# Kernel tuning notes

Hardware: AMD Instinct MI355X
Metric: run time of the kernel (lower is better)

## Reference

```python
import jax, jax.numpy as jnp
import numpy as np

N, C, T, V = 32, 64, 512, 25
CO = 64            # out_channels
C4 = CO // 4       # inter channel (conv_a/conv_d output, kc//3)
W3 = 3 * V         # unfolded node dim
BN_EPS = 1e-5


def setup_inputs() -> dict:
    key = jax.random.key(0)
    ks = jax.random.split(key, 12)
    s = 0.05
    return {
        "x": jax.random.normal(ks[0], (N, C, T, V), dtype=jnp.float32),
        "A": jax.random.uniform(ks[1], (3, W3, W3), dtype=jnp.float32) * 0.1,  # fixed adjacency buffer
        "PA": jnp.full((3, W3, W3), 1e-6, dtype=jnp.float32),                   # learned adjacency offset
        "conv_a_w": jax.random.normal(ks[2], (C4, C), dtype=jnp.float32) * s,   # 1x1 conv_a[0]
        "conv_a_b": jnp.zeros((C4,), dtype=jnp.float32),
        "conv_d_w": jax.random.normal(ks[3], (C4, C), dtype=jnp.float32) * s,   # 1x1 conv_d[0]
        "conv_d_b": jnp.zeros((C4,), dtype=jnp.float32),
        "conv_w": jax.random.normal(ks[4], (3 * C4, C), dtype=jnp.float32) * s, # main 1x1 conv (t_kernel_size=1)
        "conv_b": jnp.zeros((3 * C4,), dtype=jnp.float32),
        "out_w": jax.random.normal(ks[5], (CO, C4, 3), dtype=jnp.float32) * s,  # conv3d kernel (1,3,1)
        "out_b": jnp.zeros((CO,), dtype=jnp.float32),
        "bn_gamma": jnp.ones((CO,), dtype=jnp.float32),
        "bn_beta": jnp.zeros((CO,), dtype=jnp.float32),
        "bn_mean": jnp.zeros((CO,), dtype=jnp.float32),
        "bn_var": jnp.ones((CO,), dtype=jnp.float32),
    }


def _unfold3(x):
    # UnfoldTemporalWindows(3,1,1): (N,C,T,V) -> (N,C,T,3V), zero-pad T by 1
    n, c, t, v = x.shape
    xp = jnp.pad(x, ((0, 0), (0, 0), (1, 1), (0, 0)))
    win = jnp.stack([xp[:, :, i:i + t, :] for i in range(3)], axis=3)  # (N,C,T,3,V)
    return win.reshape(n, c, t, 3 * v)


def reference(x, A, PA, conv_a_w, conv_a_b, conv_d_w, conv_d_b,
              conv_w, conv_b, out_w, out_b, bn_gamma, bn_beta, bn_mean, bn_var):
    n, c, t, v = x.shape
    w3 = 3 * v
    Aeff = A + PA  # (3, 3V, 3V)

    x2 = _unfold3(x)  # (N,C,T,3V)

    # adaptive graph attention: matmul-softmax-matmul
    a1 = jnp.einsum('nctw,oc->notw', x2, conv_a_w) + conv_a_b[None, :, None, None]  # (N,C4,T,3V)
    a11 = a1.transpose(0, 3, 1, 2).reshape(n, w3, -1)   # (N,3V,C4*T)
    a2 = a1.reshape(n, -1, w3)                          # (N,C4*T,3V)
    att = jax.nn.softmax(jnp.matmul(a11, a2) / w3, axis=-2)  # (N,3V,3V), softmax over dim -2
    xz = jnp.matmul(x2.reshape(n, c * t, w3), att).reshape(n, c, t, w3)
    z = jnp.einsum('nctw,oc->notw', xz, conv_d_w) + conv_d_b[None, :, None, None]  # (N,C4,T,3V)

    # main branch: 1x1 conv -> split into k=3 -> einsum graph conv with A
    x1 = jnp.einsum('nctw,oc->notw', x2, conv_w) + conv_b[None, :, None, None]  # (N,3*C4,T,3V)
    c4 = conv_d_w.shape[0]
    x1 = x1.reshape(n, 3, c4, t, w3)
    x1 = jnp.einsum('nkctv,kvw->nctw', x1, Aeff)  # (N,C4,T,3V)
    x1 = x1 + z

    # conv3d (1,3,1) collapses the window-of-3 dim
    x1 = x1.reshape(n, c4, t, 3, v)
    y = jnp.einsum('nctwv,ocw->notv', x1, out_w) + out_b[None, :, None, None]  # (N,CO,T,V)

    # BatchNorm2d (inference form)
    inv = jax.lax.rsqrt(bn_var + BN_EPS)
    y = (y - bn_mean[None, :, None, None]) * (bn_gamma * inv)[None, :, None, None] + bn_beta[None, :, None, None]

    y = y + x  # in_channels == out_channels -> identity residual
    return jax.nn.relu(y)
```

## Files before the change

### kernel.cpp

```cpp
#include <hip/hip_runtime.h>
#include <hip/hip_bf16.h>


typedef unsigned short u16;
typedef unsigned int   u32;
typedef __attribute__((ext_vector_type(8))) short bf16x8;
typedef __attribute__((ext_vector_type(4))) float f32x4;

__device__ __forceinline__ float b2f(u32 u) {
    union { u32 i; float f; } x; x.i = (u & 0xffffu) << 16; return x.f;
}
__device__ __forceinline__ u16 f2b(float f) {
    union { float f; u32 i; } x; x.f = f;
    u32 i = x.i;
    return (u16)((i + 0x7fffu + ((i >> 16) & 1u)) >> 16);
}
__device__ __forceinline__ u32 pack2(float a, float b) {
    return (u32)f2b(a) | ((u32)f2b(b) << 16);
}
__device__ __forceinline__ void unpack8(uint4 u, float* f) {
    f[0] = b2f(u.x); f[1] = b2f(u.x >> 16);
    f[2] = b2f(u.y); f[3] = b2f(u.y >> 16);
    f[4] = b2f(u.z); f[5] = b2f(u.z >> 16);
    f[6] = b2f(u.w); f[7] = b2f(u.w >> 16);
}

__global__ __launch_bounds__(256) void k0_bta(
    const float* __restrict__ A, const float* __restrict__ PA,
    u16* __restrict__ BtA)
{
    int e = blockIdx.x * 256 + threadIdx.x;
    if (e >= 80 * 288) return;
    int w = e / 288, k = e - w * 288;
    int r = k >> 5, v = k & 31, g = r / 3, i = r - g * 3;
    float val = 0.f;
    if (v < 25 && w < 75) {
        int idx = (g * 75 + i * 25 + v) * 75 + w;
        val = A[idx] + PA[idx];
    }
    BtA[e] = f2b(val);
}

__global__ __launch_bounds__(256, 2) void k1_conv80(
    const float* __restrict__ x,
    const float* __restrict__ wa, const float* __restrict__ ba,
    const float* __restrict__ wd, const float* __restrict__ bd,
    const float* __restrict__ wc, const float* __restrict__ bc,
    u16* __restrict__ a1o, u16* __restrict__ hcn)
{
    __shared__ __align__(16) u16 Xt[256 * 64];
    __shared__ __align__(16) u16 Csh[80 * 264];
    char* XtB = (char*)Xt;

    const int b    = blockIdx.x;
    const int n    = b >> 4;
    const int t0   = (b & 15) << 5;
    const int tid  = threadIdx.x;
    const int wave = tid >> 6, lane = tid & 63;
    const int q    = lane >> 4, r = lane & 15;

    bf16x8 wfrag[5][2];
    float  breg[5];
    #pragma unroll
    for (int mt = 0; mt < 5; ++mt) {
        const int o = mt * 16 + r;
        const float* src = (o < 16) ? (wa + o * 64)
                         : (o < 32) ? (wd + (o - 16) * 64)
                                    : (wc + (o - 32) * 64);
        breg[mt] = (o < 16) ? ba[o] : (o < 32) ? bd[o - 16] : bc[o - 32];
        #pragma unroll
        for (int ks = 0; ks < 2; ++ks) {
            bf16x8 f;
            #pragma unroll
            for (int j = 0; j < 8; ++j)
                f[j] = (short)f2b(src[ks * 32 + q * 8 + j]);
            wfrag[mt][ks] = f;
        }
    }

    if (t0 == 0) {
        uint4 z; z.x = 0u; z.y = 0u; z.z = 0u; z.w = 0u;
        for (int e = tid; e < 50; e += 256)
            *(uint4*)&a1o[((size_t)n * 514) * 400 + e * 8] = z;
    }
    if (t0 == 480) {
        uint4 z; z.x = 0u; z.y = 0u; z.z = 0u; z.w = 0u;
        for (int e = tid; e < 50; e += 256)
            *(uint4*)&a1o[((size_t)n * 514 + 513) * 400 + e * 8] = z;
    }

    {
        uint4 z; z.x = 0u; z.y = 0u; z.z = 0u; z.w = 0u;
        for (int e = tid; e < 448; e += 256) {
            const int pc = e >> 3, ch = e & 7;
            const int tl = pc / 7, pv = pc - tl * 7;
            const int col = tl * 32 + 25 + pv;
            *(uint4*)(XtB + col * 128 + ch * 16) = z;
        }
    }

    auto epilogue = [&](int tbp) {
        for (int e = tid; e < 2048; e += 256) {
            const int cc  = e >> 5;
            const int rem = e & 31;
            const int tl  = rem >> 2, v0 = (rem & 3) << 3;
            const int o   = (cc < 48) ? cc + 32 : cc - 32;
            uint4 pk = *(const uint4*)&Csh[o * 264 + tl * 32 + v0];
            *(uint4*)&hcn[(((size_t)n * 64 + cc) * 512 + (tbp + tl)) * 32 + v0] = pk;
        }
        for (int e = tid; e < 400; e += 256) {
            const int tv = e >> 1, h = (e & 1) << 3;
            const int tl = (tv * 41) >> 10;
            const int v  = tv - tl * 25;
            const int cb = tl * 32 + v;
            u16 a[8];
            #pragma unroll
            for (int k = 0; k < 8; ++k) a[k] = Csh[(h + k) * 264 + cb];
            uint4 pk;
            pk.x = (u32)a[0] | ((u32)a[1] << 16);
            pk.y = (u32)a[2] | ((u32)a[3] << 16);
            pk.z = (u32)a[4] | ((u32)a[5] << 16);
            pk.w = (u32)a[6] | ((u32)a[7] << 16);
            *(uint4*)&a1o[(((size_t)n * 514 + (tbp + tl + 1)) * 25 + v) * 16 + h] = pk;
        }
    };

    for (int s = 0; s < 4; ++s) {
        const int tb = t0 + s * 8;

        if (s > 0) epilogue(tb - 8);
        for (int e = tid; e < 400; e += 256) {
            const int co = e / 50;
            const int tq = e - co * 50;
            const float* gp = x + (((size_t)n * 64 + co * 8) * 512 + tb) * 25 + tq * 4;
            float fl[32];
            #pragma unroll
            for (int i = 0; i < 8; ++i) {
                const float4 t4 = *(const float4*)(gp + (size_t)i * 12800);
                fl[i * 4 + 0] = t4.x; fl[i * 4 + 1] = t4.y;
                fl[i * 4 + 2] = t4.z; fl[i * 4 + 3] = t4.w;
            }
            #pragma unroll
            for (int j = 0; j < 4; ++j) {
                const int tv  = tq * 4 + j;
                const int tl  = (tv * 41) >> 10;
                const int col = tl * 32 + (tv - tl * 25);
                uint4 pk;
                pk.x = pack2(fl[0 * 4 + j], fl[1 * 4 + j]);
                pk.y = pack2(fl[2 * 4 + j], fl[3 * 4 + j]);
                pk.z = pack2(fl[4 * 4 + j], fl[5 * 4 + j]);
                pk.w = pack2(fl[6 * 4 + j], fl[7 * 4 + j]);
                *(uint4*)(XtB + col * 128 + ((co * 16) ^ ((col & 7) << 4))) = pk;
            }
        }
        __syncthreads();

        {
            f32x4 acc[4][5];
            #pragma unroll
            for (int a_ = 0; a_ < 4; ++a_)
                #pragma unroll
                for (int m_ = 0; m_ < 5; ++m_)
                    acc[a_][m_] = (f32x4){0.f, 0.f, 0.f, 0.f};

            #pragma unroll
            for (int nt4 = 0; nt4 < 4; ++nt4) {
                const int col = (wave * 4 + nt4) * 16 + r;
                const int swz = (col & 7) << 4;
                const char* rowp = (const char*)Xt + col * 128;
                const bf16x8 x0 = *(const bf16x8*)(rowp + ((q * 16) ^ swz));
                const bf16x8 x1 = *(const bf16x8*)(rowp + ((64 + q * 16) ^ swz));
                #pragma unroll
                for (int mt = 0; mt < 5; ++mt) {
                    acc[nt4][mt] = __builtin_amdgcn_mfma_f32_16x16x32_bf16(
                        x0, wfrag[mt][0], acc[nt4][mt], 0, 0, 0);
                    acc[nt4][mt] = __builtin_amdgcn_mfma_f32_16x16x32_bf16(
                        x1, wfrag[mt][1], acc[nt4][mt], 0, 0, 0);
                }
            }
            #pragma unroll
            for (int nt4 = 0; nt4 < 4; ++nt4) {
                const int colb = (wave * 4 + nt4) * 16 + q * 4;
                #pragma unroll
                for (int mt = 0; mt < 5; ++mt) {
                    const int o = mt * 16 + r;
                    const float bi = breg[mt];
                    uint2 pr;
                    pr.x = pack2(acc[nt4][mt][0] + bi, acc[nt4][mt][1] + bi);
                    pr.y = pack2(acc[nt4][mt][2] + bi, acc[nt4][mt][3] + bi);
                    *(uint2*)&Csh[o * 264 + colb] = pr;
                }
            }
        }
        __syncthreads();
    }
    epilogue(t0 + 24);
}

__global__ __launch_bounds__(256, 2) void k2a_mfma(
    const u16* __restrict__ a1o, float* __restrict__ Spart)
{
    __shared__ u16 U[80 * 136];
    __shared__ float Sred[80 * 80];
    const int b   = blockIdx.x;
    const int n   = b >> 4;
    const int tc  = b & 15;
    const int t0  = tc * 32;
    const int tid = threadIdx.x;
    const int wave = tid >> 6, lane = tid & 63;
    const int q = lane >> 4, col = lane & 15;

    f32x4 acc[25];
    #pragma unroll
    for (int i = 0; i < 25; ++i) acc[i] = (f32x4){0.f, 0.f, 0.f, 0.f};

    for (int s = 0; s < 4; ++s) {
        __syncthreads();
        for (int e = tid; e < 1280; e += 256) {
            int row = e >> 4, c8 = (e & 15) << 3;
            uint4 val; val.x = 0u; val.y = 0u; val.z = 0u; val.w = 0u;
            if (row < 75) {
                int i = row / 25, v = row - i * 25;
                int tl = c8 >> 4, o0 = c8 & 8;
                int tp = t0 + s * 8 + tl + i;
                val = *(const uint4*)&a1o[(((size_t)n * 514 + tp) * 25 + v) * 16 + o0];
            }
            *(uint4*)&U[row * 136 + c8] = val;
        }
        __syncthreads();

        const int k0 = wave * 32 + q * 8;
        bf16x8 fr[5];
        #pragma unroll
        for (int r = 0; r < 5; ++r)
            fr[r] = *(const bf16x8*)&U[(r * 16 + col) * 136 + k0];
        #pragma unroll
        for (int mt = 0; mt < 5; ++mt)
            #pragma unroll
            for (int nt = 0; nt < 5; ++nt)
                acc[mt * 5 + nt] = __builtin_amdgcn_mfma_f32_16x16x32_bf16(
                    fr[mt], fr[nt], acc[mt * 5 + nt], 0, 0, 0);
    }

    for (int w = 0; w < 4; ++w) {
        if (wave == w) {
            #pragma unroll
            for (int mt = 0; mt < 5; ++mt)
                #pragma unroll
                for (int nt = 0; nt < 5; ++nt)
                    #pragma unroll
                    for (int reg = 0; reg < 4; ++reg) {
                        int idx = (mt * 16 + q * 4 + reg) * 80 + nt * 16 + col;
                        if (w == 0) Sred[idx]  = acc[mt * 5 + nt][reg];
                        else        Sred[idx] += acc[mt * 5 + nt][reg];
                    }
        }
        __syncthreads();
    }
    float* dst = &Spart[(size_t)(n * 16 + tc) * 6400];
    for (int e = tid; e < 6400; e += 256) dst[e] = Sred[e];
}

__global__ __launch_bounds__(256) void k2b_softmax(
    const float* __restrict__ Spart, u16* __restrict__ BtT)
{
    __shared__ float S[6400];
    const int n = blockIdx.x, tid = threadIdx.x;
    for (int e = tid; e < 6400; e += 256) {
        float s = 0.f;
        for (int ks = 0; ks < 16; ++ks)
            s += Spart[(size_t)(n * 16 + ks) * 6400 + e];
        S[e] = s * (1.0f / 75.0f);
    }
    __syncthreads();
    if (tid < 80) {
        const int w2 = tid;
        float r = 0.f;
        if (w2 < 75) {
            float m = -1e30f;
            for (int w1 = 0; w1 < 75; ++w1) m = fmaxf(m, S[w1 * 80 + w2]);
            float s = 0.f;
            for (int w1 = 0; w1 < 75; ++w1) {
                float e = __expf(S[w1 * 80 + w2] - m);
                S[w1 * 80 + w2] = e;
                s += e;
            }
            r = 1.0f / s;
        }
        for (int k = 0; k < 96; ++k) {
            int i = k >> 5, v = k & 31;
            float val = (w2 < 75 && v < 25) ? S[(i * 25 + v) * 80 + w2] * r : 0.f;
            BtT[((size_t)n * 80 + w2) * 96 + k] = f2b(val);
        }
    }
}

__global__ __launch_bounds__(256, 2) void k3_graph(
    const u16* __restrict__ hcn, const u16* __restrict__ BtA,
    const u16* __restrict__ BtT, u16* __restrict__ sum12)
{
    __shared__ u16 Bt[80 * 392];
    const int b    = blockIdx.x;
    const int n    = b >> 4;
    const int tblk = (b & 15) << 5;
    const int tid  = threadIdx.x;

    for (int e = tid; e < 3840; e += 256) {
        int row = e / 48, cs = e - row * 48;
        uint4 val;
        if (cs < 36) val = *(const uint4*)&BtA[row * 288 + cs * 8];
        else         val = *(const uint4*)&BtT[((size_t)n * 80 + row) * 96 + (cs - 36) * 8];
        *(uint4*)&Bt[row * 392 + cs * 8] = val;
    }
    __syncthreads();

    const int wave = tid >> 6, lane = tid & 63;
    const int c = lane & 15, q = lane >> 4;
    const int tb = tblk + wave * 8;

    for (int tt = 0; tt < 8; tt += 2) {
        const int t0 = tb + tt, t1 = t0 + 1;
        bf16x8 a0[12], a1[12];
        #pragma unroll
        for (int r = 0; r < 12; ++r) {
            const int g = r / 3, i = r - g * 3;
            const size_t rowb = ((size_t)n * 64 + g * 16 + c) * 512;
            const int tp0 = t0 + i - 1, tp1 = t1 + i - 1;
            a0[r] = (tp0 >= 0 && tp0 < 512)
                  ? *(const bf16x8*)&hcn[(rowb + tp0) * 32 + q * 8] : (bf16x8)(short)0;
            a1[r] = (tp1 >= 0 && tp1 < 512)
                  ? *(const bf16x8*)&hcn[(rowb + tp1) * 32 + q * 8] : (bf16x8)(short)0;
        }
        #pragma unroll 1
        for (int nt = 0; nt < 5; ++nt) {
            f32x4 acc0 = {0.f, 0.f, 0.f, 0.f};
            f32x4 acc1 = {0.f, 0.f, 0.f, 0.f};
            const u16* bp = &Bt[(nt * 16 + c) * 392 + q * 8];
            #pragma unroll
            for (int r = 0; r < 12; ++r) {
                bf16x8 bf = *(const bf16x8*)(bp + r * 32);
                acc0 = __builtin_amdgcn_mfma_f32_16x16x32_bf16(a0[r], bf, acc0, 0, 0, 0);
                acc1 = __builtin_amdgcn_mfma_f32_16x16x32_bf16(a1[r], bf, acc1, 0, 0, 0);
            }
            const int w = nt * 16 + c;
            if (w < 75) {
                const int ww = (w >= 50) ? 2 : ((w >= 25) ? 1 : 0);
                const int v  = w - ww * 25;
                const size_t b0 = ((size_t)n * 512 + t0) * 1536 + v * 48 + q * 12 + ww;
                const size_t b1 = ((size_t)n * 512 + t1) * 1536 + v * 48 + q * 12 + ww;
                #pragma unroll
                for (int reg = 0; reg < 4; ++reg) {
                    sum12[b0 + (size_t)(reg * 3)] = f2b(acc0[reg]);
                    sum12[b1 + (size_t)(reg * 3)] = f2b(acc1[reg]);
                }
            }
        }
    }
}

__global__ __launch_bounds__(256, 2) void k4_out(
    const u16* __restrict__ sum12,
    const float* __restrict__ ow, const float* __restrict__ obias,
    const float* __restrict__ bg, const float* __restrict__ bb,
    const float* __restrict__ bm, const float* __restrict__ bv,
    const float* __restrict__ x, float* __restrict__ out)
{
    __shared__ __align__(16) u16 Bsh[256 * 64];
    char* BshB = (char*)Bsh;
    const int b    = blockIdx.x;
    const int n    = b >> 6;
    const int t0   = (b & 63) << 3;
    const int tid  = threadIdx.x;
    const int wave = tid >> 6, lane = tid & 63;
    const int q    = lane >> 4, c15 = lane & 15;

    {
        uint4 z; z.x = 0u; z.y = 0u; z.z = 0u; z.w = 0u;
        for (int e = tid; e < 960; e += 256) {
            int col, j;
            if (e < 512) { col = e >> 1; j = 6 + (e & 1); }
            else {
                const int r2 = e - 512;
                const int cc = r2 >> 3; j = r2 & 7;
                const int tl = cc / 7, pv = cc - tl * 7;
                col = tl * 32 + 25 + pv;
            }
            *(uint4*)(BshB + col * 128 + ((j * 16) ^ ((col & 7) << 4))) = z;
        }
    }
    for (int e = tid; e < 1200; e += 256) {
        const int j  = e % 6;
        const int rv = e / 6;
        const int tl = (rv * 41) >> 10;
        const int v  = rv - tl * 25;
        const uint4 val = *(const uint4*)
            &sum12[((size_t)n * 512 + t0 + tl) * 1536 + v * 48 + j * 8];
        const int col = tl * 32 + v;
        *(uint4*)(BshB + col * 128 + ((j * 16) ^ ((col & 7) << 4))) = val;
    }

    bf16x8 wfrag[4][2];
    #pragma unroll
    for (int mt = 0; mt < 4; ++mt) {
        const int o = mt * 16 + c15;
        #pragma unroll
        for (int ks = 0; ks < 2; ++ks) {
            bf16x8 f;
            #pragma unroll
            for (int j = 0; j < 8; ++j) {
                const int k = ks * 32 + q * 8 + j;
                f[j] = (k < 48) ? (short)f2b(ow[o * 48 + k]) : (short)0;
            }
            wfrag[mt][ks] = f;
        }
    }
    float scl[4][4], shf[4][4], obv[4][4];
    #pragma unroll
    for (int mt = 0; mt < 4; ++mt)
        #pragma unroll
        for (int reg = 0; reg < 4; ++reg) {
            const int o = mt * 16 + q * 4 + reg;
            const float s = bg[o] * rsqrtf(bv[o] + 1e-5f);
            scl[mt][reg] = s;
            shf[mt][reg] = bb[o] - bm[o] * s;
            obv[mt][reg] = obias[o];
        }
    __syncthreads();

    f32x4 acc[4][4];
    #pragma unroll
    for (int ct = 0; ct < 4; ++ct)
        #pragma unroll
        for (int mt = 0; mt < 4; ++mt)
            acc[ct][mt] = (f32x4){0.f, 0.f, 0.f, 0.f};

    const int wb = wave * 64;
    #pragma unroll
    for (int ct = 0; ct < 4; ++ct) {
        const int col = wb + ct * 16 + c15;
        const int swz = (col & 7) << 4;
        const char* rp = BshB + col * 128;
        const bf16x8 b0 = *(const bf16x8*)(rp + ((q * 16) ^ swz));
        const bf16x8 b1 = *(const bf16x8*)(rp + ((64 + q * 16) ^ swz));
        #pragma unroll
        for (int mt = 0; mt < 4; ++mt) {
            acc[ct][mt] = __builtin_amdgcn_mfma_f32_16x16x32_bf16(
                wfrag[mt][0], b0, acc[ct][mt], 0, 0, 0);
            acc[ct][mt] = __builtin_amdgcn_mfma_f32_16x16x32_bf16(
                wfrag[mt][1], b1, acc[ct][mt], 0, 0, 0);
        }
    }

    #pragma unroll
    for (int ct = 0; ct < 4; ++ct) {
        const int col = wb + ct * 16 + c15;
        const int tl = col >> 5, v = col & 31;
        if (v < 25) {
            const int t = t0 + tl;
            #pragma unroll
            for (int mt = 0; mt < 4; ++mt) {
                #pragma unroll
                for (int reg = 0; reg < 4; ++reg) {
                    const int o = mt * 16 + q * 4 + reg;
                    const size_t idx = (((size_t)n * 64 + o) * 512 + t) * 25 + v;
                    const float y = (acc[ct][mt][reg] + obv[mt][reg]) * scl[mt][reg]
                                    + shf[mt][reg] + x[idx];
                    out[idx] = fmaxf(y, 0.f);
                }
            }
        }
    }
}

extern "C" void kernel_launch(void* const* d_in, const int* in_sizes, int n_in,
                              void* d_out, int out_size, void* d_ws, size_t ws_size,
                              hipStream_t stream)
{
    const float* x  = (const float*)d_in[0];
    const float* A  = (const float*)d_in[1];
    const float* PA = (const float*)d_in[2];
    const float* wa = (const float*)d_in[3];
    const float* ba = (const float*)d_in[4];
    const float* wd = (const float*)d_in[5];
    const float* bd = (const float*)d_in[6];
    const float* wc = (const float*)d_in[7];
    const float* bc = (const float*)d_in[8];
    const float* ow = (const float*)d_in[9];
    const float* ob = (const float*)d_in[10];
    const float* bg = (const float*)d_in[11];
    const float* bb = (const float*)d_in[12];
    const float* bm = (const float*)d_in[13];
    const float* bv = (const float*)d_in[14];
    float* out = (float*)d_out;

    char* ws = (char*)d_ws;
    u16*   a1o   = (u16*)(ws);
    u16*   hcn   = (u16*)(ws + 13158400);
    u16*   sum12 = (u16*)(ws + 80267264);
    float* Spart = (float*)(ws + 80267264);
    u16*   BtA   = (u16*)(ws + 130598912);
    u16*   BtT   = (u16*)(ws + 130644992);

    k0_bta    <<<90,   256, 0, stream>>>(A, PA, BtA);
    k1_conv80 <<<512,  256, 0, stream>>>(x, wa, ba, wd, bd, wc, bc, a1o, hcn);
    k2a_mfma  <<<512,  256, 0, stream>>>(a1o, Spart);
    k2b_softmax<<<32,  256, 0, stream>>>(Spart, BtT);
    k3_graph  <<<512,  256, 0, stream>>>(hcn, BtA, BtT, sum12);
    k4_out    <<<4096 / 2, 256, 0, stream>>>(sum12, ow, ob, bg, bb, bm, bv, x, out);
}
```

Before: 470.7 us.

## Repack sum12 layout and stage k4 output through LDS for vectorized stores

The graph kernel swaps the MFMA operand order so each lane holds a channel index, and writes sum12 in a dense (v,window,channel) layout with a 1200-element row stride instead of a strided 1536 layout. The output kernel permutes its weight fragment indices to match, folds the conv bias into the BN shift, and stages results in shared memory. It then does coalesced float4 residual loads and output stores instead of scattered scalar accesses. Occupancy hint goes to 3 blocks per SM; the extra barriers and LDS transpose add some latency.

```diff
diff --git a/kernel.cpp b/kernel.cpp
--- a/kernel.cpp
+++ b/kernel.cpp
@@ -17,12 +17,6 @@
 }
 __device__ __forceinline__ u32 pack2(float a, float b) {
     return (u32)f2b(a) | ((u32)f2b(b) << 16);
-}
-__device__ __forceinline__ void unpack8(uint4 u, float* f) {
-    f[0] = b2f(u.x); f[1] = b2f(u.x >> 16);
-    f[2] = b2f(u.y); f[3] = b2f(u.y >> 16);
-    f[4] = b2f(u.z); f[5] = b2f(u.z >> 16);
-    f[6] = b2f(u.w); f[7] = b2f(u.w >> 16);
 }
 
 __global__ __launch_bounds__(256) void k0_bta(
@@ -339,34 +333,38 @@
             #pragma unroll
             for (int r = 0; r < 12; ++r) {
                 bf16x8 bf = *(const bf16x8*)(bp + r * 32);
-                acc0 = __builtin_amdgcn_mfma_f32_16x16x32_bf16(a0[r], bf, acc0, 0, 0, 0);
-                acc1 = __builtin_amdgcn_mfma_f32_16x16x32_bf16(a1[r], bf, acc1, 0, 0, 0);
-            }
-            const int w = nt * 16 + c;
-            if (w < 75) {
-                const int ww = (w >= 50) ? 2 : ((w >= 25) ? 1 : 0);
-                const int v  = w - ww * 25;
-                const size_t b0 = ((size_t)n * 512 + t0) * 1536 + v * 48 + q * 12 + ww;
-                const size_t b1 = ((size_t)n * 512 + t1) * 1536 + v * 48 + q * 12 + ww;
-                #pragma unroll
-                for (int reg = 0; reg < 4; ++reg) {
-                    sum12[b0 + (size_t)(reg * 3)] = f2b(acc0[reg]);
-                    sum12[b1 + (size_t)(reg * 3)] = f2b(acc1[reg]);
+                acc0 = __builtin_amdgcn_mfma_f32_16x16x32_bf16(bf, a0[r], acc0, 0, 0, 0);
+                acc1 = __builtin_amdgcn_mfma_f32_16x16x32_bf16(bf, a1[r], acc1, 0, 0, 0);
+            }
+            const size_t tb0 = ((size_t)n * 512 + t0) * 1200;
+            const size_t tb1 = ((size_t)n * 512 + t1) * 1200;
+            #pragma unroll
+            for (int reg = 0; reg < 4; ++reg) {
+                const int w = nt * 16 + q * 4 + reg;
+                if (w < 75) {
+                    const int ww = (w >= 50) ? 2 : ((w >= 25) ? 1 : 0);
+                    const int v  = w - ww * 25;
+                    const int off = (v * 3 + ww) * 16 + c;
+                    sum12[tb0 + off] = f2b(acc0[reg]);
+                    sum12[tb1 + off] = f2b(acc1[reg]);
                 }
             }
         }
     }
 }
 
-__global__ __launch_bounds__(256, 2) void k4_out(
+__global__ __launch_bounds__(256, 3) void k4_out(
     const u16* __restrict__ sum12,
     const float* __restrict__ ow, const float* __restrict__ obias,
     const float* __restrict__ bg, const float* __restrict__ bb,
     const float* __restrict__ bm, const float* __restrict__ bv,
     const float* __restrict__ x, float* __restrict__ out)
 {
-    __shared__ __align__(16) u16 Bsh[256 * 64];
-    char* BshB = (char*)Bsh;
+    __shared__ __align__(16) char smem[64 * 204 * 4];
+    u16*   Bsh = (u16*)smem;
+    float* Csh = (float*)smem;
+    char*  BshB = smem;
+
     const int b    = blockIdx.x;
     const int n    = b >> 6;
     const int t0   = (b & 63) << 3;
@@ -394,7 +392,7 @@
         const int tl = (rv * 41) >> 10;
         const int v  = rv - tl * 25;
         const uint4 val = *(const uint4*)
-            &sum12[((size_t)n * 512 + t0 + tl) * 1536 + v * 48 + j * 8];
+            &sum12[((size_t)n * 512 + t0 + tl) * 1200 + v * 48 + j * 8];
         const int col = tl * 32 + v;
         *(uint4*)(BshB + col * 128 + ((j * 16) ^ ((col & 7) << 4))) = val;
     }
@@ -409,21 +407,21 @@
             #pragma unroll
             for (int j = 0; j < 8; ++j) {
                 const int k = ks * 32 + q * 8 + j;
-                f[j] = (k < 48) ? (short)f2b(ow[o * 48 + k]) : (short)0;
+                const int cc = k & 15, ww = k >> 4;
+                f[j] = (k < 48) ? (short)f2b(ow[o * 48 + cc * 3 + ww]) : (short)0;
             }
             wfrag[mt][ks] = f;
         }
     }
-    float scl[4][4], shf[4][4], obv[4][4];
+    float scl[4][4], shf2[4][4];
     #pragma unroll
     for (int mt = 0; mt < 4; ++mt)
         #pragma unroll
         for (int reg = 0; reg < 4; ++reg) {
             const int o = mt * 16 + q * 4 + reg;
             const float s = bg[o] * rsqrtf(bv[o] + 1e-5f);
-            scl[mt][reg] = s;
-            shf[mt][reg] = bb[o] - bm[o] * s;
-            obv[mt][reg] = obias[o];
+            scl[mt][reg]  = s;
+            shf2[mt][reg] = bb[o] + (obias[o] - bm[o]) * s;
         }
     __syncthreads();
 
@@ -450,25 +448,37 @@
                 wfrag[mt][1], b1, acc[ct][mt], 0, 0, 0);
         }
     }
+    __syncthreads();
 
     #pragma unroll
     for (int ct = 0; ct < 4; ++ct) {
         const int col = wb + ct * 16 + c15;
         const int tl = col >> 5, v = col & 31;
         if (v < 25) {
-            const int t = t0 + tl;
-            #pragma unroll
-            for (int mt = 0; mt < 4; ++mt) {
+            const int cc = tl * 25 + v;
+            #pragma unroll
+            for (int mt = 0; mt < 4; ++mt)
                 #pragma unroll
                 for (int reg = 0; reg < 4; ++reg) {
                     const int o = mt * 16 + q * 4 + reg;
-                    const size_t idx = (((size_t)n * 64 + o) * 512 + t) * 25 + v;
-                    const float y = (acc[ct][mt][reg] + obv[mt][reg]) * scl[mt][reg]
-                                    + shf[mt][reg] + x[idx];
-                    out[idx] = fmaxf(y, 0.f);
+                    Csh[o * 204 + cc] =
+                        acc[ct][mt][reg] * scl[mt][reg] + shf2[mt][reg];
                 }
-            }
-        }
+        }
+    }
+    __syncthreads();
+
+    for (int e = tid; e < 3200; e += 256) {
+        const int o = e / 50, jj = e - o * 50;
+        const size_t gidx = (((size_t)n * 64 + o) * 512 + t0) * 25 + jj * 4;
+        const float4 xv = *(const float4*)&x[gidx];
+        const float* cp = &Csh[o * 204 + jj * 4];
+        float4 yv;
+        yv.x = fmaxf(cp[0] + xv.x, 0.f);
+        yv.y = fmaxf(cp[1] + xv.y, 0.f);
+        yv.z = fmaxf(cp[2] + xv.z, 0.f);
+        yv.w = fmaxf(cp[3] + xv.w, 0.f);
+        *(float4*)&out[gidx] = yv;
     }
 }
 
@@ -506,5 +516,5 @@
     k2a_mfma  <<<512,  256, 0, stream>>>(a1o, Spart);
     k2b_softmax<<<32,  256, 0, stream>>>(Spart, BtT);
     k3_graph  <<<512,  256, 0, stream>>>(hcn, BtA, BtT, sum12);
-    k4_out    <<<4096 / 2, 256, 0, stream>>>(sum12, ow, ob, bg, bb, bm, bv, x, out);
-}
+    k4_out    <<<2048, 256, 0, stream>>>(sum12, ow, ob, bg, bb, bm, bv, x, out);
+}
```

Result: faster. 449.1 us (-4.6%).
